# Performance work log

Hardware: AMD Instinct MI355X
Metric: run time of the kernel (lower is better)

The kernel has to match this reference:

```python
import jax, jax.numpy as jnp
import numpy as np

DIM = 768
HEADS = 12
HEAD_DIM = DIM // HEADS
SCALE = HEAD_DIM ** -0.5


def setup_inputs() -> dict:
    key = jax.random.key(0)
    ks = jax.random.split(key, 9)
    B, N, M, C = 4, 1024, 1024, DIM
    std = C ** -0.5
    return {
        "q": jax.random.normal(ks[0], (B, N, C), jnp.float32),
        "k": jax.random.normal(ks[1], (B, M, C), jnp.float32),
        "v": jax.random.normal(ks[2], (B, M, C), jnp.float32),
        "mask": jax.random.uniform(ks[3], (B, N, M), jnp.float32),
        "Wq": jax.random.normal(ks[4], (C, C), jnp.float32) * std,
        "Wk": jax.random.normal(ks[5], (C, C), jnp.float32) * std,
        "Wv": jax.random.normal(ks[6], (C, C), jnp.float32) * std,
        "Wp": jax.random.normal(ks[7], (C, C), jnp.float32) * std,
        "bp": jax.random.normal(ks[8], (C,), jnp.float32) * 0.01,
    }


def reference(q, k, v, mask, Wq, Wk, Wv, Wp, bp):
    B, N, C = q.shape
    M = k.shape[1]
    H, D = HEADS, HEAD_DIM
    qh = (q @ Wq).reshape(B, N, H, D)
    kh = (k @ Wk).reshape(B, M, H, D)
    vh = (v @ Wv).reshape(B, M, H, D)
    attn = jnp.einsum('bnhd,bmhd->bhnm', qh, kh) * SCALE
    attn = jax.nn.softmax(attn, axis=-1)
    # post-softmax multiplicative mask, broadcast over heads
    attn = attn * mask[:, None, :, :]
    x = jnp.einsum('bhnm,bmhd->bnhd', attn, vh).reshape(B, N, C)
    return x @ Wp + bp
```

## Files before the change

kernel.cpp:

```cpp
#include <hip/hip_runtime.h>

typedef __bf16 bf16x8 __attribute__((ext_vector_type(8)));
typedef float f32x4 __attribute__((ext_vector_type(4)));

__device__ __forceinline__ unsigned short f2bf(float f) {
  union { float f; unsigned u; } x; x.f = f;
  unsigned r = x.u + 0x7FFFu + ((x.u >> 16) & 1u);
  return (unsigned short)(r >> 16);
}

__device__ __forceinline__ float fast_exp2(float x) {
  float r;
  asm("v_exp_f32 %0, %1" : "=v"(r) : "v"(x));
  return r;
}

__device__ __forceinline__ void gload_lds16(const void* g, void* l) {
  __builtin_amdgcn_global_load_lds(
      (const __attribute__((address_space(1))) unsigned int*)g,
      (__attribute__((address_space(3))) unsigned int*)l, 16, 0, 0);
}

__device__ __forceinline__ f32x4 mfma16(bf16x8 a, bf16x8 b, f32x4 c) {
  return __builtin_amdgcn_mfma_f32_16x16x32_bf16(a, b, c, 0, 0, 0);
}

__device__ __forceinline__ bf16x8 pack8(const f32x4& a, const f32x4& b) {
  bf16x8 r;
  r[0] = (__bf16)a[0]; r[1] = (__bf16)a[1]; r[2] = (__bf16)a[2]; r[3] = (__bf16)a[3];
  r[4] = (__bf16)b[0]; r[5] = (__bf16)b[1]; r[6] = (__bf16)b[2]; r[7] = (__bf16)b[3];
  return r;
}

__global__ __launch_bounds__(256) void conv_all(const float* __restrict__ q,
                                                const float* __restrict__ k,
                                                const float* __restrict__ v,
                                                const float* __restrict__ W0,
                                                const float* __restrict__ W1,
                                                const float* __restrict__ W2,
                                                const float* __restrict__ W3,
                                                unsigned short* __restrict__ dst,
                                                unsigned short* __restrict__ Wt) {
  __shared__ float tile[32][33];
  if (blockIdx.y < 3) {
    const float* src = (blockIdx.y == 0) ? q : (blockIdx.y == 1 ? k : v);
    size_t i = ((size_t)blockIdx.x * 256 + threadIdx.x) * 4;
    float4 f = *(const float4*)(src + i);
    ushort4 u;
    u.x = f2bf(f.x); u.y = f2bf(f.y); u.z = f2bf(f.z); u.w = f2bf(f.w);
    *(ushort4*)(dst + (size_t)blockIdx.y * (4096u * 768u) + i) = u;
  } else {
    if (blockIdx.x >= 2304) return;
    int idx = blockIdx.x;
    int bx = idx % 24, by = (idx / 24) % 24, bz = idx / 576;
    const float* W = (bz == 0) ? W0 : (bz == 1) ? W1 : (bz == 2) ? W2 : W3;
    int tx = threadIdx.x & 31, ty = threadIdx.x >> 5;
    int n0 = bx * 32, k0 = by * 32;
#pragma unroll
    for (int i = 0; i < 4; ++i)
      tile[ty * 4 + i][tx] = W[(size_t)(k0 + ty * 4 + i) * 768 + n0 + tx];
    __syncthreads();
    unsigned short* o = Wt + (size_t)bz * 768 * 768;
#pragma unroll
    for (int i = 0; i < 4; ++i)
      o[(size_t)(n0 + ty * 4 + i) * 768 + k0 + tx] = f2bf(tile[tx][ty * 4 + i]);
  }
}

__global__ __launch_bounds__(256) void gemm_qkv(const unsigned short* __restrict__ Abase,
                                                const unsigned short* __restrict__ Wt,
                                                unsigned short* __restrict__ Hq,
                                                unsigned short* __restrict__ Hk,
                                                unsigned short* __restrict__ Hvt) {
  __shared__ unsigned short As[2][128 * 64], Bs[2][128 * 64];
  const int flat = blockIdx.x;
  const int lid = (flat & 7) * 72 + (flat >> 3);
  const int z = lid / 192;
  const int rem = lid - z * 192;
  const int m0 = (rem & 31) * 128;
  const int n0 = (rem >> 5) * 128;
  const unsigned short* A = Abase + (size_t)z * 4096 * 768;
  const unsigned short* B = Wt + (size_t)z * 768 * 768;
  const int t = threadIdx.x, l = t & 63, wid = t >> 6;
  const int g = l >> 4, c16 = l & 15;
  const int wm = (wid >> 1) * 64, wn = (wid & 1) * 64;

  auto stage = [&](unsigned short* dst, const unsigned short* src, int base, int k0) {
#pragma unroll
    for (int i = 0; i < 4; ++i) {
      int fc = i * 256 + t, r = fc >> 3, c = (fc & 7) ^ ((r >> 1) & 7);
      gload_lds16(src + (size_t)(base + r) * 768 + k0 + c * 8, (char*)dst + fc * 16);
    }
  };
  stage(As[0], A, m0, 0);
  stage(Bs[0], B, n0, 0);
  asm volatile("s_waitcnt vmcnt(0)" ::: "memory");
  __syncthreads();
  f32x4 acc[4][4] = {};
  for (int s = 0; s < 12; ++s) {
    const int cur = s & 1;
    if (s < 11) {
      stage(As[cur ^ 1], A, m0, (s + 1) * 64);
      stage(Bs[cur ^ 1], B, n0, (s + 1) * 64);
    }
#pragma unroll
    for (int kk = 0; kk < 2; ++kk) {
      const int ch = kk * 4 + g;
      bf16x8 a[4], bw[4];
#pragma unroll
      for (int mi = 0; mi < 4; ++mi) {
        int r = wm + mi * 16 + c16;
        a[mi] = *(const bf16x8*)((char*)As[cur] + r * 128 + (((ch ^ (r >> 1)) & 7) << 4));
      }
#pragma unroll
      for (int ni = 0; ni < 4; ++ni) {
        int r = wn + ni * 16 + c16;
        bw[ni] = *(const bf16x8*)((char*)Bs[cur] + r * 128 + (((ch ^ (r >> 1)) & 7) << 4));
      }
#pragma unroll
      for (int mi = 0; mi < 4; ++mi)
#pragma unroll
        for (int ni = 0; ni < 4; ++ni)
          acc[mi][ni] = mfma16(a[mi], bw[ni], acc[mi][ni]);
    }
    __syncthreads();
  }

  if (z < 2) {
    const float f = (z == 0) ? 0.125f * 1.44269504088896341f : 1.0f;
    unsigned short* C = (z == 0) ? Hq : Hk;
#pragma unroll
    for (int mi = 0; mi < 4; ++mi)
#pragma unroll
      for (int ni = 0; ni < 4; ++ni) {
        int col = n0 + wn + ni * 16 + c16;
        int row = m0 + wm + mi * 16 + g * 4;
#pragma unroll
        for (int j = 0; j < 4; ++j)
          C[(size_t)(row + j) * 768 + col] = f2bf(acc[mi][ni][j] * f);
      }
  } else {
#pragma unroll
    for (int mi = 0; mi < 4; ++mi) {
      int rowbase = m0 + wm + mi * 16;
      int bat = rowbase >> 10;
      int mloc = (rowbase & 1023) + g * 4;
#pragma unroll
      for (int ni = 0; ni < 4; ++ni) {
        int col = n0 + wn + ni * 16 + c16;
        ushort4 u;
        u.x = f2bf(acc[mi][ni][0]); u.y = f2bf(acc[mi][ni][1]);
        u.z = f2bf(acc[mi][ni][2]); u.w = f2bf(acc[mi][ni][3]);
        *(ushort4*)(Hvt + (((size_t)(bat * 768 + col)) << 10) + mloc) = u;
      }
    }
  }
}

__global__ __launch_bounds__(256) void attn(const unsigned short* __restrict__ qh,
                                            const unsigned short* __restrict__ kh,
                                            const unsigned short* __restrict__ vhT,
                                            const float* __restrict__ mask,
                                            unsigned short* __restrict__ xb) {
  __shared__ unsigned short Ks[3][64 * 64], Vts[3][64 * 64];
  const int flat = blockIdx.x;
  const int lid = (flat & 7) * 96 + (flat >> 3);
  const int h = lid % 12, qt = (lid / 12) & 15, b = lid / 192;
  const int t = threadIdx.x, l = t & 63, wid = t >> 6;
  const int g = l >> 4, c16 = l & 15;

  const unsigned short* qp =
      qh + ((size_t)(b * 1024 + qt * 64 + wid * 16 + c16)) * 768 + h * 64 + g * 8;
  bf16x8 aq0 = *(const bf16x8*)qp;
  bf16x8 aq1 = *(const bf16x8*)(qp + 32);

  const int fc0 = t, r0 = fc0 >> 3, c0 = (fc0 & 7) ^ ((r0 >> 1) & 7);
  const int fc1 = 256 + t, r1 = fc1 >> 3, c1 = (fc1 & 7) ^ ((r1 >> 1) & 7);
  const int s0 = 32 * (r0 >> 5) + 8 * ((r0 >> 2) & 3) + 4 * ((r0 >> 4) & 1) + (r0 & 3);
  const int s1 = 32 * (r1 >> 5) + 8 * ((r1 >> 2) & 3) + 4 * ((r1 >> 4) & 1) + (r1 & 3);
  const unsigned short* kp0 = kh + (size_t)(b * 1024 + s0) * 768 + h * 64 + c0 * 8;
  const unsigned short* kp1 = kh + (size_t)(b * 1024 + s1) * 768 + h * 64 + c1 * 8;
  const unsigned short* vp0 = vhT + ((size_t)(b * 768 + h * 64 + r0)) * 1024 + c0 * 8;
  const unsigned short* vp1 = vhT + ((size_t)(b * 768 + h * 64 + r1)) * 1024 + c1 * 8;

  auto stageKV = [&](int buf) {
    char* kd = (char*)Ks[buf];
    char* vd = (char*)Vts[buf];
    gload_lds16(kp0, kd + fc0 * 16);
    gload_lds16(kp1, kd + fc1 * 16);
    gload_lds16(vp0, vd + fc0 * 16);
    gload_lds16(vp1, vd + fc1 * 16);
    kp0 += 64 * 768; kp1 += 64 * 768; vp0 += 64; vp1 += 64;
  };

  const float* mq = mask + ((size_t)(b * 1024 + qt * 64 + wid * 16 + c16)) * 1024 + 8 * g;

  stageKV(0);
  stageKV(1);
  asm volatile("s_waitcnt vmcnt(4)" ::: "memory");
  __builtin_amdgcn_s_barrier();

  f32x4 o[4] = {};
  f32x4 ls = {0.f, 0.f, 0.f, 0.f};

  for (int kv = 0; kv < 16; ++kv) {
    const int cur = kv % 3;
    if (kv < 14) stageKV((kv + 2) % 3);
    const float* mk = mq + kv * 64;
    f32x4 mreg[4];
    mreg[0] = *(const f32x4*)(mk);
    mreg[1] = *(const f32x4*)(mk + 4);
    mreg[2] = *(const f32x4*)(mk + 32);
    mreg[3] = *(const f32x4*)(mk + 36);
    f32x4 p[4] = {};
#pragma unroll
    for (int kk = 0; kk < 2; ++kk) {
      const int ch = kk * 4 + g;
      bf16x8 aq = kk ? aq1 : aq0;
#pragma unroll
      for (int ni = 0; ni < 4; ++ni) {
        int r = ni * 16 + c16;
        bf16x8 bk = *(const bf16x8*)((char*)Ks[cur] + r * 128 + (((ch ^ (r >> 1)) & 7) << 4));
        p[ni] = mfma16(bk, aq, p[ni]);
      }
    }
#pragma unroll
    for (int ni = 0; ni < 4; ++ni) {
      float e0 = fast_exp2(p[ni][0]);
      float e1 = fast_exp2(p[ni][1]);
      float e2 = fast_exp2(p[ni][2]);
      float e3 = fast_exp2(p[ni][3]);
      ls[ni] += (e0 + e1) + (e2 + e3);
      p[ni][0] = e0 * mreg[ni][0];
      p[ni][1] = e1 * mreg[ni][1];
      p[ni][2] = e2 * mreg[ni][2];
      p[ni][3] = e3 * mreg[ni][3];
    }
    bf16x8 pa0 = pack8(p[0], p[1]);
    bf16x8 pa1 = pack8(p[2], p[3]);
#pragma unroll
    for (int kk = 0; kk < 2; ++kk) {
      const int ch = kk * 4 + g;
      bf16x8 ap = kk ? pa1 : pa0;
#pragma unroll
      for (int ni = 0; ni < 4; ++ni) {
        int r = ni * 16 + c16;
        bf16x8 bv = *(const bf16x8*)((char*)Vts[cur] + r * 128 + (((ch ^ (r >> 1)) & 7) << 4));
        o[ni] = mfma16(ap, bv, o[ni]);
      }
    }
    if (kv < 14) {
      asm volatile("s_waitcnt vmcnt(4)" ::: "memory");
      __builtin_amdgcn_s_barrier();
    } else if (kv == 14) {
      asm volatile("s_waitcnt vmcnt(0)" ::: "memory");
      __builtin_amdgcn_s_barrier();
    }
  }
  float s = (ls[0] + ls[1]) + (ls[2] + ls[3]);
  s += __shfl_xor(s, 16);
  s += __shfl_xor(s, 32);
  float rinv = 1.0f / s;
  const int rb = (l & 48) | ((l >> 2) & 12);
  float rj[4];
#pragma unroll
  for (int j = 0; j < 4; ++j) rj[j] = __shfl(rinv, rb + j);
#pragma unroll
  for (int ni = 0; ni < 4; ++ni) {
    int col = h * 64 + ni * 16 + c16;
    int row = qt * 64 + wid * 16 + g * 4;
#pragma unroll
    for (int j = 0; j < 4; ++j)
      xb[((size_t)(b * 1024) + row + j) * 768 + col] = f2bf(o[ni][j] * rj[j]);
  }
}

__global__ __launch_bounds__(256) void gemm_proj(const unsigned short* __restrict__ A,
                                                 const unsigned short* __restrict__ B,
                                                 const float* __restrict__ bias,
                                                 float* __restrict__ C) {
  __shared__ unsigned short As[2][64 * 64], Bs[2][64 * 64];
  const int flat = blockIdx.x;
  const int lid = (flat & 7) * 96 + (flat >> 3);
  const int m0 = (lid & 63) * 64;
  const int n0 = (lid >> 6) * 64;
  const int t = threadIdx.x, l = t & 63, wid = t >> 6;
  const int g = l >> 4, c16 = l & 15;
  const int wm = (wid >> 1) * 32, wn = (wid & 1) * 32;
  auto stage = [&](unsigned short* dst, const unsigned short* src, int base, int k0) {
#pragma unroll
    for (int i = 0; i < 2; ++i) {
      int fc = i * 256 + t, r = fc >> 3, c = (fc & 7) ^ ((r >> 1) & 7);
      gload_lds16(src + (size_t)(base + r) * 768 + k0 + c * 8, (char*)dst + fc * 16);
    }
  };
  stage(As[0], A, m0, 0);
  stage(Bs[0], B, n0, 0);
  asm volatile("s_waitcnt vmcnt(0)" ::: "memory");
  __syncthreads();
  f32x4 acc[2][2] = {};
  for (int s = 0; s < 12; ++s) {
    const int cur = s & 1;
    if (s < 11) {
      stage(As[cur ^ 1], A, m0, (s + 1) * 64);
      stage(Bs[cur ^ 1], B, n0, (s + 1) * 64);
    }
#pragma unroll
    for (int kk = 0; kk < 2; ++kk) {
      const int ch = kk * 4 + g;
      bf16x8 a[2], bw[2];
#pragma unroll
      for (int mi = 0; mi < 2; ++mi) {
        int r = wm + mi * 16 + c16;
        a[mi] = *(const bf16x8*)((char*)As[cur] + r * 128 + (((ch ^ (r >> 1)) & 7) << 4));
      }
#pragma unroll
      for (int ni = 0; ni < 2; ++ni) {
        int r = wn + ni * 16 + c16;
        bw[ni] = *(const bf16x8*)((char*)Bs[cur] + r * 128 + (((ch ^ (r >> 1)) & 7) << 4));
      }
#pragma unroll
      for (int mi = 0; mi < 2; ++mi)
#pragma unroll
        for (int ni = 0; ni < 2; ++ni)
          acc[mi][ni] = mfma16(a[mi], bw[ni], acc[mi][ni]);
    }
    __syncthreads();
  }
#pragma unroll
  for (int mi = 0; mi < 2; ++mi)
#pragma unroll
    for (int ni = 0; ni < 2; ++ni) {
      int col = n0 + wn + ni * 16 + c16;
      int row = m0 + wm + mi * 16 + g * 4;
      float bv = bias[col];
#pragma unroll
      for (int j = 0; j < 4; ++j)
        C[(size_t)(row + j) * 768 + col] = acc[mi][ni][j] + bv;
    }
}

extern "C" void kernel_launch(void* const* d_in, const int* in_sizes, int n_in,
                              void* d_out, int out_size, void* d_ws, size_t ws_size,
                              hipStream_t stream) {
  const float* q    = (const float*)d_in[0];
  const float* k    = (const float*)d_in[1];
  const float* v    = (const float*)d_in[2];
  const float* mask = (const float*)d_in[3];
  const float* Wq   = (const float*)d_in[4];
  const float* Wk   = (const float*)d_in[5];
  const float* Wv   = (const float*)d_in[6];
  const float* Wp   = (const float*)d_in[7];
  const float* bp   = (const float*)d_in[8];
  float* out = (float*)d_out;

  const size_t MN = (size_t)4096 * 768;
  const size_t WW = (size_t)768 * 768;
  unsigned short* qkv_bf = (unsigned short*)d_ws;
  unsigned short* wt     = qkv_bf + 3 * MN;
  unsigned short* heads  = wt + 4 * WW;
  unsigned short* xb     = heads + 3 * MN;

  conv_all<<<dim3(3072, 4), 256, 0, stream>>>(q, k, v, Wq, Wk, Wv, Wp, qkv_bf, wt);
  gemm_qkv<<<dim3(576), 256, 0, stream>>>(qkv_bf, wt, heads, heads + MN, heads + 2 * MN);
  attn<<<dim3(768), 256, 0, stream>>>(heads, heads + MN, heads + 2 * MN, mask, xb);
  gemm_proj<<<dim3(768), 256, 0, stream>>>(xb, wt + 3 * WW, bp, out);
}
```

Measured before the change: 92.71 us.

## Split attention KV range in two blocks and merge partial results

Splits each attention tile's 1024-key range into two halves processed by separate blocks, doubling the grid to 1536 blocks for better occupancy across CUs. Each half writes unnormalized bf16 partial outputs and row sums, and a new merge kernel adds them and normalizes. The KV pipeline drops from triple to double buffering with full waits. This adds a kernel launch, extra global traffic for the partials and an extra bf16 rounding step. It reuses the qkv_bf workspace region for the partials.

```diff
diff --git a/kernel.cpp b/kernel.cpp
--- a/kernel.cpp
+++ b/kernel.cpp
@@ -7,6 +7,11 @@
   union { float f; unsigned u; } x; x.f = f;
   unsigned r = x.u + 0x7FFFu + ((x.u >> 16) & 1u);
   return (unsigned short)(r >> 16);
+}
+
+__device__ __forceinline__ float bf2f(unsigned short v) {
+  union { unsigned u; float f; } x; x.u = (unsigned)v << 16;
+  return x.f;
 }
 
 __device__ __forceinline__ float fast_exp2(float x) {
@@ -161,11 +166,14 @@
                                             const unsigned short* __restrict__ kh,
                                             const unsigned short* __restrict__ vhT,
                                             const float* __restrict__ mask,
-                                            unsigned short* __restrict__ xb) {
-  __shared__ unsigned short Ks[3][64 * 64], Vts[3][64 * 64];
+                                            unsigned short* __restrict__ opb,
+                                            float* __restrict__ lsp) {
+  __shared__ unsigned short Ks[2][64 * 64], Vts[2][64 * 64];
   const int flat = blockIdx.x;
-  const int lid = (flat & 7) * 96 + (flat >> 3);
-  const int h = lid % 12, qt = (lid / 12) & 15, b = lid / 192;
+  const int lid = (flat & 7) * 192 + (flat >> 3);
+  const int h = lid % 12, qt = (lid / 12) & 15;
+  const int hf = (lid / 192) & 1, b = lid / 384;
+  const int kvb = hf * 8;
   const int t = threadIdx.x, l = t & 63, wid = t >> 6;
   const int g = l >> 4, c16 = l & 15;
 
@@ -178,10 +186,10 @@
   const int fc1 = 256 + t, r1 = fc1 >> 3, c1 = (fc1 & 7) ^ ((r1 >> 1) & 7);
   const int s0 = 32 * (r0 >> 5) + 8 * ((r0 >> 2) & 3) + 4 * ((r0 >> 4) & 1) + (r0 & 3);
   const int s1 = 32 * (r1 >> 5) + 8 * ((r1 >> 2) & 3) + 4 * ((r1 >> 4) & 1) + (r1 & 3);
-  const unsigned short* kp0 = kh + (size_t)(b * 1024 + s0) * 768 + h * 64 + c0 * 8;
-  const unsigned short* kp1 = kh + (size_t)(b * 1024 + s1) * 768 + h * 64 + c1 * 8;
-  const unsigned short* vp0 = vhT + ((size_t)(b * 768 + h * 64 + r0)) * 1024 + c0 * 8;
-  const unsigned short* vp1 = vhT + ((size_t)(b * 768 + h * 64 + r1)) * 1024 + c1 * 8;
+  const unsigned short* kp0 = kh + (size_t)(b * 1024 + kvb * 64 + s0) * 768 + h * 64 + c0 * 8;
+  const unsigned short* kp1 = kh + (size_t)(b * 1024 + kvb * 64 + s1) * 768 + h * 64 + c1 * 8;
+  const unsigned short* vp0 = vhT + ((size_t)(b * 768 + h * 64 + r0)) * 1024 + kvb * 64 + c0 * 8;
+  const unsigned short* vp1 = vhT + ((size_t)(b * 768 + h * 64 + r1)) * 1024 + kvb * 64 + c1 * 8;
 
   auto stageKV = [&](int buf) {
     char* kd = (char*)Ks[buf];
@@ -193,19 +201,19 @@
     kp0 += 64 * 768; kp1 += 64 * 768; vp0 += 64; vp1 += 64;
   };
 
-  const float* mq = mask + ((size_t)(b * 1024 + qt * 64 + wid * 16 + c16)) * 1024 + 8 * g;
+  const float* mq = mask + ((size_t)(b * 1024 + qt * 64 + wid * 16 + c16)) * 1024 +
+                    kvb * 64 + 8 * g;
 
   stageKV(0);
-  stageKV(1);
-  asm volatile("s_waitcnt vmcnt(4)" ::: "memory");
+  asm volatile("s_waitcnt vmcnt(0)" ::: "memory");
   __builtin_amdgcn_s_barrier();
 
   f32x4 o[4] = {};
   f32x4 ls = {0.f, 0.f, 0.f, 0.f};
 
-  for (int kv = 0; kv < 16; ++kv) {
-    const int cur = kv % 3;
-    if (kv < 14) stageKV((kv + 2) % 3);
+  for (int kv = 0; kv < 8; ++kv) {
+    const int cur = kv & 1;
+    if (kv < 7) stageKV(cur ^ 1);
     const float* mk = mq + kv * 64;
     f32x4 mreg[4];
     mreg[0] = *(const f32x4*)(mk);
@@ -249,30 +257,47 @@
         o[ni] = mfma16(ap, bv, o[ni]);
       }
     }
-    if (kv < 14) {
-      asm volatile("s_waitcnt vmcnt(4)" ::: "memory");
-      __builtin_amdgcn_s_barrier();
-    } else if (kv == 14) {
+    if (kv < 7) {
       asm volatile("s_waitcnt vmcnt(0)" ::: "memory");
       __builtin_amdgcn_s_barrier();
     }
   }
+
   float s = (ls[0] + ls[1]) + (ls[2] + ls[3]);
   s += __shfl_xor(s, 16);
   s += __shfl_xor(s, 32);
-  float rinv = 1.0f / s;
-  const int rb = (l & 48) | ((l >> 2) & 12);
-  float rj[4];
-#pragma unroll
-  for (int j = 0; j < 4; ++j) rj[j] = __shfl(rinv, rb + j);
+  if (l < 16)
+    lsp[(size_t)hf * 49152 + (((size_t)b * 12 + h) << 10) + qt * 64 + wid * 16 + l] = s;
+  unsigned short* op = opb + (size_t)hf * (4096u * 768u);
 #pragma unroll
   for (int ni = 0; ni < 4; ++ni) {
     int col = h * 64 + ni * 16 + c16;
     int row = qt * 64 + wid * 16 + g * 4;
 #pragma unroll
     for (int j = 0; j < 4; ++j)
-      xb[((size_t)(b * 1024) + row + j) * 768 + col] = f2bf(o[ni][j] * rj[j]);
-  }
+      op[((size_t)(b * 1024) + row + j) * 768 + col] = f2bf(o[ni][j]);
+  }
+}
+
+__global__ __launch_bounds__(256) void merge_halves(const unsigned short* __restrict__ op0,
+                                                    const unsigned short* __restrict__ op1,
+                                                    const float* __restrict__ lsp,
+                                                    unsigned short* __restrict__ xb) {
+  size_t i4 = ((size_t)blockIdx.x * 256 + threadIdx.x) * 4;
+  ushort4 a = *(const ushort4*)(op0 + i4);
+  ushort4 c = *(const ushort4*)(op1 + i4);
+  int row = (int)(i4 / 768);
+  int col = (int)(i4 - (size_t)row * 768);
+  int h = col >> 6;
+  int bb = row >> 10, r = row & 1023;
+  size_t li = (((size_t)bb * 12 + h) << 10) + r;
+  float rinv = 1.0f / (lsp[li] + lsp[49152 + li]);
+  ushort4 u;
+  u.x = f2bf((bf2f(a.x) + bf2f(c.x)) * rinv);
+  u.y = f2bf((bf2f(a.y) + bf2f(c.y)) * rinv);
+  u.z = f2bf((bf2f(a.z) + bf2f(c.z)) * rinv);
+  u.w = f2bf((bf2f(a.w) + bf2f(c.w)) * rinv);
+  *(ushort4*)(xb + i4) = u;
 }
 
 __global__ __launch_bounds__(256) void gemm_proj(const unsigned short* __restrict__ A,
@@ -357,12 +382,15 @@
   const size_t MN = (size_t)4096 * 768;
   const size_t WW = (size_t)768 * 768;
   unsigned short* qkv_bf = (unsigned short*)d_ws;
+  unsigned short* op     = qkv_bf;
   unsigned short* wt     = qkv_bf + 3 * MN;
   unsigned short* heads  = wt + 4 * WW;
   unsigned short* xb     = heads + 3 * MN;
+  float*          lsp    = (float*)(xb + MN);
 
   conv_all<<<dim3(3072, 4), 256, 0, stream>>>(q, k, v, Wq, Wk, Wv, Wp, qkv_bf, wt);
   gemm_qkv<<<dim3(576), 256, 0, stream>>>(qkv_bf, wt, heads, heads + MN, heads + 2 * MN);
-  attn<<<dim3(768), 256, 0, stream>>>(heads, heads + MN, heads + 2 * MN, mask, xb);
+  attn<<<dim3(1536), 256, 0, stream>>>(heads, heads + MN, heads + 2 * MN, mask, op, lsp);
+  merge_halves<<<dim3(3072), 256, 0, stream>>>(op, op + MN, lsp, xb);
   gemm_proj<<<dim3(768), 256, 0, stream>>>(xb, wt + 3 * WW, bp, out);
 }
```

New measurement: 103.7 us. 1.12x slower.
